# Kernel tuning notes

Hardware: AMD Instinct MI355X
Metric: run time of the kernel (lower is better)

Reference implementation:

```python
import jax, jax.numpy as jnp
import numpy as np

B, S, H, N = 2, 2048, 1024, 16
D = H // N


def setup_inputs() -> dict:
    key = jax.random.key(0)
    k1, k2, k3 = jax.random.split(key, 3)
    # Xavier-uniform-ish init for projection weights
    lim_in = (6.0 / (H + 3 * H)) ** 0.5
    lim_out = (6.0 / (H + H)) ** 0.5
    return {
        "hidden_states": jax.random.normal(k1, (B, S, H), dtype=jnp.float32),
        "w_in": jax.random.uniform(k2, (3 * H, H), minval=-lim_in, maxval=lim_in, dtype=jnp.float32),
        "b_in": jnp.zeros((3 * H,), dtype=jnp.float32),
        "w_out": jax.random.uniform(k3, (H, H), minval=-lim_out, maxval=lim_out, dtype=jnp.float32),
        "b_out": jnp.zeros((H,), dtype=jnp.float32),
    }


def reference(hidden_states, w_in, b_in, w_out, b_out):
    b, s, h = hidden_states.shape
    qkv = hidden_states @ w_in.T + b_in  # [B,S,3H]
    q, k, v = jnp.split(qkv, 3, axis=-1)
    # [B,S,H] -> [B,N,S,D]
    def to_heads(x):
        return x.reshape(b, s, N, D).transpose(0, 2, 1, 3)
    q, k, v = to_heads(q), to_heads(k), to_heads(v)
    scale = D ** -0.5
    scores = jnp.einsum("bnqd,bnkd->bnqk", q, k) * scale  # [B,N,S,S]
    causal = jnp.triu(jnp.ones((s, s), dtype=bool), k=1)
    scores = jnp.where(causal, -jnp.inf, scores)
    attn = jax.nn.softmax(scores, axis=-1)
    out = jnp.einsum("bnqk,bnkd->bnqd", attn, v)  # [B,N,S,D]
    out = out.transpose(0, 2, 1, 3).reshape(b, s, h)
    return out @ w_out.T + b_out
```

## Files before the change

### kernel.cpp

```cpp
#include <hip/hip_runtime.h>
#include <hip/hip_bf16.h>

#define BB 2
#define SS 2048
#define HH 1024
#define NH 16
#define DD 64
#define H3 3072
#define MM (BB*SS)

typedef unsigned short u16;
typedef unsigned int u32;
typedef __attribute__((ext_vector_type(8))) short bf16x8;
typedef __attribute__((ext_vector_type(4))) float f32x4;

__device__ __forceinline__ u16 f2bf(float f) {
    union { float f; u32 u; } v; v.f = f;
    u32 u = v.u;
    u += 0x7fffu + ((u >> 16) & 1u);
    return (u16)(u >> 16);
}
__device__ __forceinline__ float bf2f(u16 h) {
    union { u32 u; float f; } v; v.u = ((u32)h) << 16;
    return v.f;
}
__device__ __forceinline__ u32 pack2bf(float a, float b) {
    __hip_bfloat162 h = __float22bfloat162_rn(float2{a, b});
    u32 u; __builtin_memcpy(&u, &h, 4);
    return u;
}
__device__ __forceinline__ void gl_lds16(const void* g, void* l) {
    __builtin_amdgcn_global_load_lds(
        (const __attribute__((address_space(1))) u32*)g,
        (__attribute__((address_space(3))) u32*)l, 16, 0, 0);
}
__device__ __forceinline__ int ginv(int R) {
    return (R & 35) | ((R & 8) << 1) | ((R & 4) << 1) | ((R & 16) >> 2);
}

__global__ void cvt3bf(const float4* __restrict__ s0, uint2* __restrict__ d0, int n0,
                       const float4* __restrict__ s1, uint2* __restrict__ d1, int n1,
                       const float4* __restrict__ s2, uint2* __restrict__ d2, int n2) {
    int i = blockIdx.x * blockDim.x + threadIdx.x;
    const int tot = n0 + n1 + n2;
    for (; i < tot; i += gridDim.x * blockDim.x) {
        const float4* s; uint2* d; int j;
        if (i < n0)            { s = s0; d = d0; j = i; }
        else if (i < n0 + n1)  { s = s1; d = d1; j = i - n0; }
        else                   { s = s2; d = d2; j = i - n0 - n1; }
        float4 v = s[j];
        uint2 o; o.x = pack2bf(v.x, v.y); o.y = pack2bf(v.z, v.w);
        d[j] = o;
    }
}

template<int BN, int MODE>
__global__ __launch_bounds__(256, 2)
void gemm_k2(const u16* __restrict__ A, const u16* __restrict__ Bbf,
             const u16* __restrict__ biasbf, void* __restrict__ Cptr,
             u16* __restrict__ Qo, u16* __restrict__ Ko, u16* __restrict__ Vto,
             int M, int Nn, int K)
{
    constexpr int NFR = BN / 32;
    __shared__ __align__(16) u16 Alds[128 * 32];
    __shared__ __align__(16) u16 Blds[BN * 32];
    const int tid = threadIdx.x;
    const int w = tid >> 6, lane = tid & 63, quad = lane >> 4, l16 = lane & 15;
    const int m0 = blockIdx.x * 128, n0 = blockIdx.y * BN;
    const int wm = w >> 1, wn = w & 1;
    const int rA4 = lane >> 2, c8b = (lane & 3) * 8;

    f32x4 acc[4][NFR] = {};

    for (int k0 = 0; k0 < K; k0 += 32) {
        __syncthreads();
#pragma unroll
        for (int q = 0; q < 2; ++q) {
            int row0 = w * 32 + q * 16;
            gl_lds16(&A[(size_t)(m0 + row0 + rA4) * K + k0 + c8b], &Alds[row0 * 32]);
        }
#pragma unroll
        for (int q = 0; q < BN / 64; ++q) {
            int row0 = w * (BN / 4) + q * 16;
            gl_lds16(&Bbf[(size_t)(n0 + row0 + rA4) * K + k0 + c8b], &Blds[row0 * 32]);
        }
        __syncthreads();

        bf16x8 af[4], bfr[NFR];
#pragma unroll
        for (int mi = 0; mi < 4; ++mi)
            af[mi] = *(const bf16x8*)&Alds[(wm * 64 + mi * 16 + l16) * 32 + quad * 8];
#pragma unroll
        for (int ni = 0; ni < NFR; ++ni)
            bfr[ni] = *(const bf16x8*)&Blds[(wn * (BN / 2) + ni * 16 + l16) * 32 + quad * 8];
#pragma unroll
        for (int mi = 0; mi < 4; ++mi)
#pragma unroll
            for (int ni = 0; ni < NFR; ++ni)
                acc[mi][ni] = __builtin_amdgcn_mfma_f32_16x16x32_bf16(
                    af[mi], bfr[ni], acc[mi][ni], 0, 0, 0);
    }

#pragma unroll
    for (int mi = 0; mi < 4; ++mi) {
        int row_b = m0 + wm * 64 + mi * 16 + quad * 4;
#pragma unroll
        for (int ni = 0; ni < NFR; ++ni) {
            int col = n0 + wn * (BN / 2) + ni * 16 + l16;
            float bv = bf2f(biasbf[col]);
            if constexpr (MODE == 1) {
#pragma unroll
                for (int i = 0; i < 4; ++i)
                    ((float*)Cptr)[(size_t)(row_b + i) * Nn + col] = acc[mi][ni][i] + bv;
            } else {
                if (col < 1024) {
#pragma unroll
                    for (int i = 0; i < 4; ++i)
                        Qo[(size_t)(row_b + i) * 1024 + col] =
                            f2bf((acc[mi][ni][i] + bv) * 0.125f);
                } else if (col < 2048) {
#pragma unroll
                    for (int i = 0; i < 4; ++i)
                        Ko[(size_t)(row_b + i) * 1024 + (col - 1024)] =
                            f2bf(acc[mi][ni][i] + bv);
                } else {
                    int d = col - 2048, hh = d >> 6, dd = d & 63;
                    int b = row_b >> 11, s = row_b & 2047;
                    u16 t0 = f2bf(acc[mi][ni][0] + bv), t1 = f2bf(acc[mi][ni][1] + bv);
                    u16 t2 = f2bf(acc[mi][ni][2] + bv), t3 = f2bf(acc[mi][ni][3] + bv);
                    uint2 pk; pk.x = (u32)t0 | ((u32)t1 << 16);
                    pk.y = (u32)t2 | ((u32)t3 << 16);
                    *(uint2*)&Vto[((size_t)((b * 16 + hh) * 64 + dd)) * 2048 + s] = pk;
                }
            }
        }
    }
}

__global__ __launch_bounds__(256, 2)
void attn_v5(const u16* __restrict__ Q, const u16* __restrict__ Kb,
             const u16* __restrict__ Vt, u16* __restrict__ attn_out) {
    const int bid = blockIdx.x;
    const int r8 = bid & 7, qq = bid >> 3;
    const int pr = qq >> 2, g = (qq & 3) * 8 + r8;
    const int h = g & 15, b = g >> 4;
    const int tid = threadIdx.x;
    const int w = tid >> 6, lane = tid & 63, quad = lane >> 4, l16 = lane & 15;
    __shared__ __align__(16) u16 Klds[2][64 * 64];
    __shared__ __align__(16) u16 Vlds[2][64 * 64];

    const int sl = lane >> 3, cch = lane & 7;
    const int rho0 = (2 * w) * 8 + sl, rho1 = (2 * w + 1) * 8 + sl;
    const int gcs = (cch ^ sl) * 8;
    const int kg0 = ginv(rho0), kg1 = ginv(rho1);
    const int ls0 = (2 * w) * 512, ls1 = (2 * w + 1) * 512;
    const int xk0 = (quad ^ (l16 & 7)) * 8;
    const int xk1 = ((quad + 4) ^ (l16 & 7)) * 8;

    for (int half = 0; half < 2; ++half) {
        const int qt = half ? pr : (31 - pr);
        const int q0 = qt * 64;
        const int T = qt + 1;

        const u16* Qb = Q  + (size_t)(b * SS + q0) * 1024 + h * 64;
        const u16* Kg = Kb + (size_t)(b * SS) * 1024 + h * 64;
        const u16* Vg = Vt + (size_t)((b * 16 + h) * 64) * 2048;

#define STAGE_T(kv0_, bi_) do {                                               \
        gl_lds16(&Kg[(size_t)((kv0_) + kg0) * 1024 + gcs], &Klds[bi_][ls0]);  \
        gl_lds16(&Kg[(size_t)((kv0_) + kg1) * 1024 + gcs], &Klds[bi_][ls1]);  \
        gl_lds16(&Vg[(size_t)rho0 * 2048 + (kv0_) + gcs], &Vlds[bi_][ls0]);   \
        gl_lds16(&Vg[(size_t)rho1 * 2048 + (kv0_) + gcs], &Vlds[bi_][ls1]);   \
    } while (0)

        bf16x8 qf0 = *(const bf16x8*)&Qb[(size_t)(w * 16 + l16) * 1024 + quad * 8];
        bf16x8 qf1 = *(const bf16x8*)&Qb[(size_t)(w * 16 + l16) * 1024 + 32 + quad * 8];

        f32x4 oacc[4] = {};
        float lp = 0.f;

        __syncthreads();
        STAGE_T(0, 0);

        for (int t = 0; t < T; ++t) {
            const int cur = t & 1;
            __syncthreads();
            if (t + 1 < T) STAGE_T((t + 1) * 64, cur ^ 1);
            const u16* Kc = Klds[cur];
            const u16* Vc = Vlds[cur];
            f32x4 sacc[4] = {};
#pragma unroll
            for (int ni = 0; ni < 4; ++ni) {
                const int rb = (ni * 16 + l16) * 64;
                bf16x8 kf0 = *(const bf16x8*)&Kc[rb + xk0];
                bf16x8 kf1 = *(const bf16x8*)&Kc[rb + xk1];
                sacc[ni] = __builtin_amdgcn_mfma_f32_16x16x32_bf16(kf0, qf0, sacc[ni], 0, 0, 0);
                sacc[ni] = __builtin_amdgcn_mfma_f32_16x16x32_bf16(kf1, qf1, sacc[ni], 0, 0, 0);
            }
            u32 pk[4][2];
            if (t + 1 < T) {
#pragma unroll
                for (int ni = 0; ni < 4; ++ni) {
                    float p0 = __expf(sacc[ni][0]), p1 = __expf(sacc[ni][1]);
                    float p2 = __expf(sacc[ni][2]), p3 = __expf(sacc[ni][3]);
                    lp += (p0 + p1) + (p2 + p3);
                    pk[ni][0] = pack2bf(p0, p1);
                    pk[ni][1] = pack2bf(p2, p3);
                }
            } else {
                const int thr = w * 16 + l16;
#pragma unroll
                for (int ni = 0; ni < 4; ++ni) {
                    const int pb = 32 * (ni >> 1) + 8 * quad + 4 * (ni & 1);
                    float pv[4];
#pragma unroll
                    for (int i = 0; i < 4; ++i) {
                        float e = __expf(sacc[ni][i]);
                        pv[i] = (pb + i <= thr) ? e : 0.f;
                    }
                    lp += (pv[0] + pv[1]) + (pv[2] + pv[3]);
                    pk[ni][0] = pack2bf(pv[0], pv[1]);
                    pk[ni][1] = pack2bf(pv[2], pv[3]);
                }
            }
            union { u32 u[4]; bf16x8 v; } pf0, pf1;
            pf0.u[0] = pk[0][0]; pf0.u[1] = pk[0][1];
            pf0.u[2] = pk[1][0]; pf0.u[3] = pk[1][1];
            pf1.u[0] = pk[2][0]; pf1.u[1] = pk[2][1];
            pf1.u[2] = pk[3][0]; pf1.u[3] = pk[3][1];
#pragma unroll
            for (int ni = 0; ni < 4; ++ni) {
                const int rb = (ni * 16 + l16) * 64;
                bf16x8 vf0 = *(const bf16x8*)&Vc[rb + xk0];
                bf16x8 vf1 = *(const bf16x8*)&Vc[rb + xk1];
                oacc[ni] = __builtin_amdgcn_mfma_f32_16x16x32_bf16(pf0.v, vf0, oacc[ni], 0, 0, 0);
                oacc[ni] = __builtin_amdgcn_mfma_f32_16x16x32_bf16(pf1.v, vf1, oacc[ni], 0, 0, 0);
            }
        }

        lp += __shfl_xor(lp, 16, 64);
        lp += __shfl_xor(lp, 32, 64);
        float linv[4];
#pragma unroll
        for (int i = 0; i < 4; ++i)
            linv[i] = 1.0f / __shfl(lp, quad * 4 + i, 64);

        u16* ob = attn_out + (size_t)(b * SS + q0 + w * 16) * 1024 + h * 64;
#pragma unroll
        for (int ni = 0; ni < 4; ++ni)
#pragma unroll
            for (int i = 0; i < 4; ++i)
                ob[(size_t)(quad * 4 + i) * 1024 + ni * 16 + l16] =
                    f2bf(oacc[ni][i] * linv[i]);
#undef STAGE_T
    }
}

extern "C" void kernel_launch(void* const* d_in, const int* in_sizes, int n_in,
                              void* d_out, int out_size, void* d_ws, size_t ws_size,
                              hipStream_t stream) {
    const float* hidden = (const float*)d_in[0];
    const float* w_in   = (const float*)d_in[1];
    const float* b_in   = (const float*)d_in[2];
    const float* w_out  = (const float*)d_in[3];
    const float* b_out  = (const float*)d_in[4];
    float* out = (float*)d_out;

    char* ws = (char*)d_ws;
    u16* hid_bf  = (u16*)d_out;
    u16* wi_bf   = (u16*)ws;
    u16* bi_bf   = (u16*)(ws + 6291456);
    u16* attn_ws = (u16*)ws;
    u16* Qbuf    = (u16*)(ws + 8388608);
    u16* wo_bf   = (u16*)(ws + 8388608);
    u16* bo_bf   = (u16*)(ws + 8388608 + 2097152);
    u16* Kbuf    = (u16*)(ws + 16777216);
    u16* Vtbuf   = (u16*)(ws + 25165824);

    cvt3bf<<<dim3(2048), dim3(256), 0, stream>>>(
        (const float4*)hidden, (uint2*)hid_bf, 1048576,
        (const float4*)w_in,   (uint2*)wi_bf,  786432,
        (const float4*)b_in,   (uint2*)bi_bf,  768);
    gemm_k2<128, 2><<<dim3(32, 24), dim3(256), 0, stream>>>(
        hid_bf, wi_bf, bi_bf, nullptr, Qbuf, Kbuf, Vtbuf, MM, H3, HH);
    attn_v5<<<dim3(512), dim3(256), 0, stream>>>(
        Qbuf, Kbuf, Vtbuf, attn_ws);
    cvt3bf<<<dim3(512), dim3(256), 0, stream>>>(
        (const float4*)w_out, (uint2*)wo_bf, 262144,
        (const float4*)b_out, (uint2*)bo_bf, 256,
        nullptr, nullptr, 0);
    gemm_k2<64, 1><<<dim3(32, 16), dim3(256), 0, stream>>>(
        attn_ws, wo_bf, bo_bf, out, nullptr, nullptr, nullptr, MM, HH, HH);
}
```

Measured before the change: 177.2 us.

## Double-buffer LDS tiles in GEMM and raise occupancy hint to three

The GEMM kernel now uses two LDS buffers for the A and B tiles. It issues the global-to-LDS loads for the next K-slice before running the MFMAs on the current slice, so load latency can overlap with compute and there is one barrier per iteration instead of two. The launch bounds also move from 2 to 3 blocks per CU. That caps registers per thread, which may cause spills given the large accumulator array, while LDS use per block doubles.

```diff
diff --git a/kernel.cpp b/kernel.cpp
--- a/kernel.cpp
+++ b/kernel.cpp
@@ -55,15 +55,15 @@
 }
 
 template<int BN, int MODE>
-__global__ __launch_bounds__(256, 2)
+__global__ __launch_bounds__(256, 3)
 void gemm_k2(const u16* __restrict__ A, const u16* __restrict__ Bbf,
              const u16* __restrict__ biasbf, void* __restrict__ Cptr,
              u16* __restrict__ Qo, u16* __restrict__ Ko, u16* __restrict__ Vto,
              int M, int Nn, int K)
 {
     constexpr int NFR = BN / 32;
-    __shared__ __align__(16) u16 Alds[128 * 32];
-    __shared__ __align__(16) u16 Blds[BN * 32];
+    __shared__ __align__(16) u16 Alds[2][128 * 32];
+    __shared__ __align__(16) u16 Blds[2][BN * 32];
     const int tid = threadIdx.x;
     const int w = tid >> 6, lane = tid & 63, quad = lane >> 4, l16 = lane & 15;
     const int m0 = blockIdx.x * 128, n0 = blockIdx.y * BN;
@@ -72,27 +72,35 @@
 
     f32x4 acc[4][NFR] = {};
 
-    for (int k0 = 0; k0 < K; k0 += 32) {
+#define GSTAGE(k0_, bi_) do {                                                  \
+    _Pragma("unroll")                                                          \
+    for (int q = 0; q < 2; ++q) {                                              \
+        int row0 = w * 32 + q * 16;                                            \
+        gl_lds16(&A[(size_t)(m0 + row0 + rA4) * K + (k0_) + c8b],              \
+                 &Alds[bi_][row0 * 32]);                                       \
+    }                                                                          \
+    _Pragma("unroll")                                                          \
+    for (int q = 0; q < BN / 64; ++q) {                                        \
+        int row0 = w * (BN / 4) + q * 16;                                      \
+        gl_lds16(&Bbf[(size_t)(n0 + row0 + rA4) * K + (k0_) + c8b],            \
+                 &Blds[bi_][row0 * 32]);                                       \
+    }                                                                          \
+} while (0)
+
+    const int NT = K >> 5;
+    GSTAGE(0, 0);
+    for (int t = 0; t < NT; ++t) {
+        const int cur = t & 1;
         __syncthreads();
-#pragma unroll
-        for (int q = 0; q < 2; ++q) {
-            int row0 = w * 32 + q * 16;
-            gl_lds16(&A[(size_t)(m0 + row0 + rA4) * K + k0 + c8b], &Alds[row0 * 32]);
-        }
-#pragma unroll
-        for (int q = 0; q < BN / 64; ++q) {
-            int row0 = w * (BN / 4) + q * 16;
-            gl_lds16(&Bbf[(size_t)(n0 + row0 + rA4) * K + k0 + c8b], &Blds[row0 * 32]);
-        }
-        __syncthreads();
+        if (t + 1 < NT) GSTAGE((t + 1) << 5, cur ^ 1);
 
         bf16x8 af[4], bfr[NFR];
 #pragma unroll
         for (int mi = 0; mi < 4; ++mi)
-            af[mi] = *(const bf16x8*)&Alds[(wm * 64 + mi * 16 + l16) * 32 + quad * 8];
+            af[mi] = *(const bf16x8*)&Alds[cur][(wm * 64 + mi * 16 + l16) * 32 + quad * 8];
 #pragma unroll
         for (int ni = 0; ni < NFR; ++ni)
-            bfr[ni] = *(const bf16x8*)&Blds[(wn * (BN / 2) + ni * 16 + l16) * 32 + quad * 8];
+            bfr[ni] = *(const bf16x8*)&Blds[cur][(wn * (BN / 2) + ni * 16 + l16) * 32 + quad * 8];
 #pragma unroll
         for (int mi = 0; mi < 4; ++mi)
 #pragma unroll
@@ -100,6 +108,7 @@
                 acc[mi][ni] = __builtin_amdgcn_mfma_f32_16x16x32_bf16(
                     af[mi], bfr[ni], acc[mi][ni], 0, 0, 0);
     }
+#undef GSTAGE
 
 #pragma unroll
     for (int mi = 0; mi < 4; ++mi) {
```

Result: no change. 173.9 us (-1.9%).
